# Optimization experiments

Measured on AMD Instinct MI355X. Metric: run time of the kernel, lower is better.

## Reference

```python
import jax, jax.numpy as jnp
import numpy as np

N = 100000      # nodes
E = 1600000     # edges (avg degree 16)
DIN = 48        # input features
H = 48          # hidden
DOUT = 16       # output classes


def setup_inputs() -> dict:
    key = jax.random.key(0)
    ks = jax.random.split(key, 20)
    inp = {
        "x": jax.random.normal(ks[0], (N, DIN), jnp.float32),
        "edge_index": jax.random.randint(ks[1], (2, E), 0, N, jnp.int32),
    }
    # (name, in_dim, out_dim) for the 2-layer MLP in each of 3 GINConvs + final fc
    layers = [("11", DIN, H), ("12", H, H),
              ("21", H, H), ("22", H, H),
              ("31", H, H), ("32", H, H),
              ("f1", H, H), ("f2", H, DOUT)]
    for i, (nm, din, dout) in enumerate(layers):
        inp["w" + nm] = jax.random.normal(ks[2 + i], (din, dout), jnp.float32) / np.float32(np.sqrt(din))
        inp["b" + nm] = jax.random.normal(ks[10 + i], (dout,), jnp.float32) * 0.01
    return inp


def reference(x, edge_index, w11, b11, w12, b12, w21, b21, w22, b22,
              w31, b31, w32, b32, wf1, bf1, wf2, bf2):
    src, dst = edge_index[0], edge_index[1]
    n = x.shape[0]

    def gin_conv(h, w1, b1, w2, b2):
        # scatter-sum neighbor aggregation: sum_{j in N(i)} h_j
        agg = jax.ops.segment_sum(h[src], dst, num_segments=n)  # [N, d]
        h2 = h + agg  # eps = 0 (PyG GINConv default): (1+eps)*x + agg
        h2 = jax.nn.relu(h2 @ w1 + b1)
        return jax.nn.relu(h2 @ w2 + b2)

    h = gin_conv(x, w11, b11, w12, b12)
    h = gin_conv(h, w21, b21, w22, b22)
    h = gin_conv(h, w31, b31, w32, b32)
    # final fc head: Linear -> ReLU -> Linear
    return jax.nn.relu(h @ wf1 + bf1) @ wf2 + bf2
```

## Files before the change

### kernel.cpp

```cpp
#include <hip/hip_runtime.h>

#define NN 100000
#define NE 1600000
#define D 48
#define BK_SHIFT 8
#define BK_NODES 256
#define NBK 391
#define CAP 5120
#define EPB 4096
#define NBINB 391
#define NG 1563
#define CAPG 1344
#define ST 72

typedef _Float16 f16x8 __attribute__((ext_vector_type(8)));
typedef float f32x4 __attribute__((ext_vector_type(4)));


__global__ __launch_bounds__(256) void prepbin(
    const int* __restrict__ src, const int* __restrict__ dst,
    int* __restrict__ bucketLen, int* __restrict__ arena,
    const float* __restrict__ x,
    const float* __restrict__ w11, const float* __restrict__ w12,
    const float* __restrict__ w21, const float* __restrict__ w22,
    const float* __restrict__ w31, const float* __restrict__ w32,
    const float* __restrict__ wf1, const float* __restrict__ wf2,
    _Float16* __restrict__ wp, uint4* __restrict__ outh) {
    __shared__ int sCnt[NBK];
    __shared__ int sBase[NBK];
    int b = blockIdx.x;
    int tid = threadIdx.x;
    if (b < NBINB) {
        for (int i = tid; i < NBK; i += 256) sCnt[i] = 0;
        __syncthreads();
        int e0 = b * EPB;
        int eend = e0 + EPB;
        if (eend > NE) eend = NE;
        for (int i = e0 + tid; i < eend; i += 256) atomicAdd(&sCnt[dst[i] >> BK_SHIFT], 1);
        __syncthreads();
        int rot = (b * 101) % NBK;
        for (int k = tid; k < NBK; k += 256) {
            int i = k + rot;
            if (i >= NBK) i -= NBK;
            int v = sCnt[i];
            sBase[i] = v ? atomicAdd(&bucketLen[i], v) : 0;
        }
        __syncthreads();
        for (int i = tid; i < NBK; i += 256) sCnt[i] = 0;
        __syncthreads();
        for (int i = e0 + tid; i < eend; i += 256) {
            int d = dst[i];
            int bk = d >> BK_SHIFT;
            int off = atomicAdd(&sCnt[bk], 1) + sBase[bk];
            if (off < CAP) arena[(size_t)bk * CAP + off] = ((d & (BK_NODES - 1)) << 17) | src[i];
        }
    } else if (b < NBINB + 8) {
        int l = b - NBINB;
        const float* W;
        int NL = 48;
        switch (l) {
            case 0: W = w11; break;
            case 1: W = w12; break;
            case 2: W = w21; break;
            case 3: W = w22; break;
            case 4: W = w31; break;
            case 5: W = w32; break;
            case 6: W = wf1; break;
            default: W = wf2; NL = 16; break;
        }
        _Float16* T = wp + l * 3072;
        int total = 64 * NL;
        for (int i = tid; i < total; i += 256) {
            int j = i & 7;
            int m = i >> 3;
            int g = m / NL;
            int nn = m - g * NL;
            int k = g * 8 + j;
            T[i] = (k < 48) ? (_Float16)W[k * NL + nn] : (_Float16)0.f;
        }
    } else {
        int i = (b - NBINB - 8) * 256 + tid;
        if (i < NN * 6) {
            const float4* p = (const float4*)(x + (size_t)i * 8);
            float4 a = p[0], bb = p[1];
            union { _Float16 h[8]; uint4 u; } pk;
            pk.h[0] = (_Float16)a.x; pk.h[1] = (_Float16)a.y;
            pk.h[2] = (_Float16)a.z; pk.h[3] = (_Float16)a.w;
            pk.h[4] = (_Float16)bb.x; pk.h[5] = (_Float16)bb.y;
            pk.h[6] = (_Float16)bb.z; pk.h[7] = (_Float16)bb.w;
            outh[i] = pk.u;
        }
    }
}


__global__ __launch_bounds__(256) void csr64(
    const int* __restrict__ arena, const int* __restrict__ bucketLen,
    int* __restrict__ rowptr, int* __restrict__ gEnd, int* __restrict__ colidx) {
    __shared__ int sCnt[64];
    __shared__ int sPos[64];
    int g = blockIdx.x;
    int tid = threadIdx.x;
    int parent = g >> 2;
    int quarter = g & 3;
    int plen = bucketLen[parent];
    if (plen > CAP) plen = CAP;
    const int* slice = arena + (size_t)parent * CAP;
    int gBase = g * CAPG;

    if (tid < 64) sCnt[tid] = 0;
    __syncthreads();
    for (int i = tid; i < plen; i += 256) {
        int p = slice[i];
        if ((p >> 23) == quarter) atomicAdd(&sCnt[(p >> 17) & 63], 1);
    }
    __syncthreads();
    if (tid < 64) {
        int v = sCnt[tid];
        int xx = v;
#pragma unroll
        for (int off = 1; off < 64; off <<= 1) {
            int y = __shfl_up(xx, off);
            if (tid >= off) xx += y;
        }
        int excl = xx - v;
        if (excl > CAPG) excl = CAPG;
        int node = (g << 6) + tid;
        if (node < NN) rowptr[node] = gBase + excl;
        sPos[tid] = gBase + excl;
        if (tid == 63) {
            int tot = xx > CAPG ? CAPG : xx;
            gEnd[g] = gBase + tot;
        }
    }
    __syncthreads();
    int lim = gBase + CAPG;
    for (int i = tid; i < plen; i += 256) {
        int p = slice[i];
        if ((p >> 23) == quarter) {
            int slot = atomicAdd(&sPos[(p >> 17) & 63], 1);
            if (slot < lim) colidx[slot] = p & 0x1FFFF;
        }
    }
}


__device__ __forceinline__ void mfma_layer48(
    const _Float16* __restrict__ wp, const float* __restrict__ bias,
    const _Float16* src, _Float16* dst, int lane) {
    int am = lane & 15, q = lane >> 4;
    f16x8 a0 = *(const f16x8*)(src + am * ST + q * 8);
    f16x8 a1 = *(const f16x8*)(src + am * ST + 32 + q * 8);
#pragma unroll
    for (int t = 0; t < 3; ++t) {
        f16x8 b0 = *(const f16x8*)(wp + ((q) * 48 + t * 16 + am) * 8);
        f16x8 b1 = *(const f16x8*)(wp + ((4 + q) * 48 + t * 16 + am) * 8);
        float bv = bias[t * 16 + am];
        f32x4 c = {bv, bv, bv, bv};
        c = __builtin_amdgcn_mfma_f32_16x16x32_f16(a0, b0, c, 0, 0, 0);
        c = __builtin_amdgcn_mfma_f32_16x16x32_f16(a1, b1, c, 0, 0, 0);
#pragma unroll
        for (int r = 0; r < 4; ++r) {
            float v = fmaxf(c[r], 0.f);
            dst[(q * 4 + r) * ST + t * 16 + am] = (_Float16)v;
        }
    }
}


__device__ __forceinline__ void gather_stage(const uint4* __restrict__ hin4,
                                             const int* __restrict__ rowptr,
                                             const int* __restrict__ col,
                                             int gend,
                                             _Float16* s0, _Float16* s1,
                                             int base, int wv, int lane, int n) {
    for (int i = lane; i < 16 * 3; i += 64) {
        int r = i / 3, cq = i % 3;
        *(uint4*)(s0 + r * ST + 48 + cq * 8) = make_uint4(0u, 0u, 0u, 0u);
        *(uint4*)(s1 + r * ST + 48 + cq * 8) = make_uint4(0u, 0u, 0u, 0u);
    }
    int s = lane & 7;
    int c = lane >> 3;
    bool act = (c < 6);
    int cc = act ? c : 0;
    int nb = base + wv * 16;
    for (int nl = 0; nl < 16; nl += 2) {
        int node0 = nb + nl;
        int node1 = node0 + 1;
        int r1 = wv * 16 + nl + 1;
        f16x8 acc0 = {0, 0, 0, 0, 0, 0, 0, 0};
        f16x8 acc1 = {0, 0, 0, 0, 0, 0, 0, 0};
        int e00 = 0, e01 = 0, e10 = 0, e11 = 0;
        if (node0 < n) {
            e00 = rowptr[node0];
            e01 = rowptr[node0 + 1];
        }
        if (node1 < n) {
            e10 = e01;
            e11 = (r1 == 63 || node1 == n - 1) ? gend : rowptr[node1 + 1];
        }
        if (act) {
            int ebA = e00, ebB = e10;
            while (ebA < e01 || ebB < e11) {
                int eA0 = ebA + s, eA1 = ebA + 8 + s;
                int eB0 = ebB + s, eB1 = ebB + 8 + s;
                bool okA0 = eA0 < e01, okA1 = eA1 < e01;
                bool okB0 = eB0 < e11, okB1 = eB1 < e11;
                int iA0 = col[okA0 ? eA0 : e00] & 0x1FFFF;
                int iA1 = col[okA1 ? eA1 : e00] & 0x1FFFF;
                int iB0 = col[okB0 ? eB0 : e10] & 0x1FFFF;
                int iB1 = col[okB1 ? eB1 : e10] & 0x1FFFF;
                uint4 vA0 = hin4[(size_t)iA0 * 6 + cc];
                uint4 vA1 = hin4[(size_t)iA1 * 6 + cc];
                uint4 vB0 = hin4[(size_t)iB0 * 6 + cc];
                uint4 vB1 = hin4[(size_t)iB1 * 6 + cc];
                if (!okA0) vA0 = make_uint4(0u, 0u, 0u, 0u);
                if (!okA1) vA1 = make_uint4(0u, 0u, 0u, 0u);
                if (!okB0) vB0 = make_uint4(0u, 0u, 0u, 0u);
                if (!okB1) vB1 = make_uint4(0u, 0u, 0u, 0u);
                acc0 += *(const f16x8*)&vA0;
                acc0 += *(const f16x8*)&vA1;
                acc1 += *(const f16x8*)&vB0;
                acc1 += *(const f16x8*)&vB1;
                ebA += 16;
                ebB += 16;
            }
        }
        union { f16x8 f; int i[4]; } a0, a1, bx;
        a0.f = acc0;
        a1.f = acc1;
#pragma unroll
        for (int m = 1; m <= 4; m <<= 1) {
            bx.i[0] = __shfl_xor(a0.i[0], m);
            bx.i[1] = __shfl_xor(a0.i[1], m);
            bx.i[2] = __shfl_xor(a0.i[2], m);
            bx.i[3] = __shfl_xor(a0.i[3], m);
            a0.f += bx.f;
            bx.i[0] = __shfl_xor(a1.i[0], m);
            bx.i[1] = __shfl_xor(a1.i[1], m);
            bx.i[2] = __shfl_xor(a1.i[2], m);
            bx.i[3] = __shfl_xor(a1.i[3], m);
            a1.f += bx.f;
        }
        if (s == 0 && act) {
            union { f16x8 f; uint4 u; } r0u, r1u;
            r0u.f = (f16x8){0, 0, 0, 0, 0, 0, 0, 0};
            r1u.f = (f16x8){0, 0, 0, 0, 0, 0, 0, 0};
            if (node0 < n) {
                uint4 self = hin4[(size_t)node0 * 6 + c];
                r0u.f = a0.f + *(const f16x8*)&self;
            }
            if (node1 < n) {
                uint4 self = hin4[(size_t)node1 * 6 + c];
                r1u.f = a1.f + *(const f16x8*)&self;
            }
            *(uint4*)(s0 + nl * ST + c * 8) = r0u.u;
            *(uint4*)(s0 + (nl + 1) * ST + c * 8) = r1u.u;
        }
    }
    __builtin_amdgcn_wave_barrier();
}

__global__ __launch_bounds__(256) void conv_fused(
    const uint4* __restrict__ hin4, const int* __restrict__ rowptr,
    const int* __restrict__ col, const int* __restrict__ gEnd,
    const _Float16* __restrict__ wp1, const float* __restrict__ B1,
    const _Float16* __restrict__ wp2, const float* __restrict__ B2,
    _Float16* __restrict__ hout, int n) {
    __shared__ __align__(16) _Float16 HA[2 * 64 * ST];
    int tid = threadIdx.x;
    int g = blockIdx.x;
    int base = g << 6;
    int lane = tid & 63;
    int wv = tid >> 6;
    _Float16* s0 = HA + wv * 16 * ST;
    _Float16* s1 = HA + 64 * ST + wv * 16 * ST;

    int gend = gEnd[g];

    gather_stage(hin4, rowptr, col, gend, s0, s1, base, wv, lane, n);
    mfma_layer48(wp1, B1, s0, s1, lane);
    __builtin_amdgcn_wave_barrier();

    int am = lane & 15, q = lane >> 4;
    f16x8 a0 = *(const f16x8*)(s1 + am * ST + q * 8);
    f16x8 a1 = *(const f16x8*)(s1 + am * ST + 32 + q * 8);
    int g0 = base + wv * 16;
#pragma unroll
    for (int t = 0; t < 3; ++t) {
        f16x8 b0 = *(const f16x8*)(wp2 + ((q) * 48 + t * 16 + am) * 8);
        f16x8 b1 = *(const f16x8*)(wp2 + ((4 + q) * 48 + t * 16 + am) * 8);
        float bv = B2[t * 16 + am];
        f32x4 c = {bv, bv, bv, bv};
        c = __builtin_amdgcn_mfma_f32_16x16x32_f16(a0, b0, c, 0, 0, 0);
        c = __builtin_amdgcn_mfma_f32_16x16x32_f16(a1, b1, c, 0, 0, 0);
#pragma unroll
        for (int r = 0; r < 4; ++r) {
            int node = g0 + q * 4 + r;
            if (node < n) {
                float v = fmaxf(c[r], 0.f);
                hout[(size_t)node * D + t * 16 + am] = (_Float16)v;
            }
        }
    }
}

__global__ __launch_bounds__(256) void tail_fused(
    const uint4* __restrict__ hin4, const int* __restrict__ rowptr,
    const int* __restrict__ col, const int* __restrict__ gEnd,
    const _Float16* __restrict__ wp1, const float* __restrict__ B1,
    const _Float16* __restrict__ wp2, const float* __restrict__ B2,
    const _Float16* __restrict__ wp3, const float* __restrict__ B3,
    const _Float16* __restrict__ wp4, const float* __restrict__ B4,
    float* __restrict__ out, int n) {
    __shared__ __align__(16) _Float16 HA[2 * 64 * ST];
    int tid = threadIdx.x;
    int g = blockIdx.x;
    int base = g << 6;
    int lane = tid & 63;
    int wv = tid >> 6;
    _Float16* s0 = HA + wv * 16 * ST;
    _Float16* s1 = HA + 64 * ST + wv * 16 * ST;

    int gend = gEnd[g];

    gather_stage(hin4, rowptr, col, gend, s0, s1, base, wv, lane, n);
    mfma_layer48(wp1, B1, s0, s1, lane);
    __builtin_amdgcn_wave_barrier();
    mfma_layer48(wp2, B2, s1, s0, lane);
    __builtin_amdgcn_wave_barrier();
    mfma_layer48(wp3, B3, s0, s1, lane);
    __builtin_amdgcn_wave_barrier();

    int am = lane & 15, q = lane >> 4;
    f16x8 a0 = *(const f16x8*)(s1 + am * ST + q * 8);
    f16x8 a1 = *(const f16x8*)(s1 + am * ST + 32 + q * 8);
    f16x8 b0 = *(const f16x8*)(wp4 + ((q) * 16 + am) * 8);
    f16x8 b1 = *(const f16x8*)(wp4 + ((4 + q) * 16 + am) * 8);
    float bv = B4[am];
    f32x4 c = {bv, bv, bv, bv};
    c = __builtin_amdgcn_mfma_f32_16x16x32_f16(a0, b0, c, 0, 0, 0);
    c = __builtin_amdgcn_mfma_f32_16x16x32_f16(a1, b1, c, 0, 0, 0);
    int g0 = base + wv * 16;
#pragma unroll
    for (int r = 0; r < 4; ++r) {
        int node = g0 + q * 4 + r;
        if (node < n) out[(size_t)node * 16 + am] = c[r];
    }
}


extern "C" void kernel_launch(void* const* d_in, const int* in_sizes, int n_in,
                              void* d_out, int out_size, void* d_ws, size_t ws_size,
                              hipStream_t stream) {
    const int n = NN, e = NE;
    const float* x = (const float*)d_in[0];
    const int* ei = (const int*)d_in[1];
    const int* src = ei;
    const int* dst = ei + e;
    const float* w11 = (const float*)d_in[2];
    const float* b11 = (const float*)d_in[3];
    const float* w12 = (const float*)d_in[4];
    const float* b12 = (const float*)d_in[5];
    const float* w21 = (const float*)d_in[6];
    const float* b21 = (const float*)d_in[7];
    const float* w22 = (const float*)d_in[8];
    const float* b22 = (const float*)d_in[9];
    const float* w31 = (const float*)d_in[10];
    const float* b31 = (const float*)d_in[11];
    const float* w32 = (const float*)d_in[12];
    const float* b32 = (const float*)d_in[13];
    const float* wf1 = (const float*)d_in[14];
    const float* bf1 = (const float*)d_in[15];
    const float* wf2 = (const float*)d_in[16];
    const float* bf2 = (const float*)d_in[17];
    float* out = (float*)d_out;

    uint4* HAa = (uint4*)d_ws;
    uint4* HAb = HAa + (size_t)n * 6;
    _Float16* WP = (_Float16*)(HAb + (size_t)n * 6);
    int* rowptr = (int*)(WP + 8 * 3072);
    int* gEnd = rowptr + n;
    int* colidx = gEnd + NG;
    int* arena = colidx + (size_t)NG * CAPG;
    int* bucketLen = arena + (size_t)NBK * CAP;
    size_t needed = (size_t)((char*)(bucketLen + NBK) - (char*)d_ws);
    if (needed > ws_size) return;

    const _Float16* wp11 = WP + 0 * 3072;
    const _Float16* wp12 = WP + 1 * 3072;
    const _Float16* wp21 = WP + 2 * 3072;
    const _Float16* wp22 = WP + 3 * 3072;
    const _Float16* wp31 = WP + 4 * 3072;
    const _Float16* wp32 = WP + 5 * 3072;
    const _Float16* wpf1 = WP + 6 * 3072;
    const _Float16* wpf2 = WP + 7 * 3072;

    hipMemsetAsync(bucketLen, 0, NBK * sizeof(int), stream);
    int gPB = NBINB + 8 + (n * 6 + 255) / 256;
    prepbin<<<gPB, 256, 0, stream>>>(src, dst, bucketLen, arena, x,
                                     w11, w12, w21, w22, w31, w32, wf1, wf2,
                                     WP, HAa);
    csr64<<<NG, 256, 0, stream>>>(arena, bucketLen, rowptr, gEnd, colidx);

    int gConv = NG;

    conv_fused<<<gConv, 256, 0, stream>>>(HAa, rowptr, colidx, gEnd,
                                          wp11, b11, wp12, b12, (_Float16*)HAb, n);
    conv_fused<<<gConv, 256, 0, stream>>>(HAb, rowptr, colidx, gEnd,
                                          wp21, b21, wp22, b22, (_Float16*)HAa, n);
    tail_fused<<<gConv, 256, 0, stream>>>(HAa, rowptr, colidx, gEnd,
                                          wp31, b31, wp32, b32,
                                          wpf1, bf1, wpf2, bf2, out, n);
}
```

Baseline: 271.4 us.

## Fuse CSR construction into first GIN conv kernel using LDS column list

Removes the separate csr64 kernel and builds each 64-node group's CSR slice inside the first conv kernel, keeping the column list and row offsets in shared memory for that layer's gather. The kernel still writes rowptr, gEnd and colidx to global memory for the later layers. This saves one kernel launch and the global round-trip of colidx/rowptr for layer 1. In exchange it adds about 5.6KB of LDS per block and extra block-level syncs, which may lower occupancy of the first conv.

```diff
diff --git a/kernel.cpp b/kernel.cpp
--- a/kernel.cpp
+++ b/kernel.cpp
@@ -94,57 +94,6 @@
 }
 
 
-__global__ __launch_bounds__(256) void csr64(
-    const int* __restrict__ arena, const int* __restrict__ bucketLen,
-    int* __restrict__ rowptr, int* __restrict__ gEnd, int* __restrict__ colidx) {
-    __shared__ int sCnt[64];
-    __shared__ int sPos[64];
-    int g = blockIdx.x;
-    int tid = threadIdx.x;
-    int parent = g >> 2;
-    int quarter = g & 3;
-    int plen = bucketLen[parent];
-    if (plen > CAP) plen = CAP;
-    const int* slice = arena + (size_t)parent * CAP;
-    int gBase = g * CAPG;
-
-    if (tid < 64) sCnt[tid] = 0;
-    __syncthreads();
-    for (int i = tid; i < plen; i += 256) {
-        int p = slice[i];
-        if ((p >> 23) == quarter) atomicAdd(&sCnt[(p >> 17) & 63], 1);
-    }
-    __syncthreads();
-    if (tid < 64) {
-        int v = sCnt[tid];
-        int xx = v;
-#pragma unroll
-        for (int off = 1; off < 64; off <<= 1) {
-            int y = __shfl_up(xx, off);
-            if (tid >= off) xx += y;
-        }
-        int excl = xx - v;
-        if (excl > CAPG) excl = CAPG;
-        int node = (g << 6) + tid;
-        if (node < NN) rowptr[node] = gBase + excl;
-        sPos[tid] = gBase + excl;
-        if (tid == 63) {
-            int tot = xx > CAPG ? CAPG : xx;
-            gEnd[g] = gBase + tot;
-        }
-    }
-    __syncthreads();
-    int lim = gBase + CAPG;
-    for (int i = tid; i < plen; i += 256) {
-        int p = slice[i];
-        if ((p >> 23) == quarter) {
-            int slot = atomicAdd(&sPos[(p >> 17) & 63], 1);
-            if (slot < lim) colidx[slot] = p & 0x1FFFF;
-        }
-    }
-}
-
-
 __device__ __forceinline__ void mfma_layer48(
     const _Float16* __restrict__ wp, const float* __restrict__ bias,
     const _Float16* src, _Float16* dst, int lane) {
@@ -168,12 +117,13 @@
 }
 
 
-__device__ __forceinline__ void gather_stage(const uint4* __restrict__ hin4,
-                                             const int* __restrict__ rowptr,
-                                             const int* __restrict__ col,
-                                             int gend,
-                                             _Float16* s0, _Float16* s1,
-                                             int base, int wv, int lane, int n) {
+template <bool LDSCOL>
+__device__ __forceinline__ void gather_core(const uint4* __restrict__ hin4,
+                                            const int* col,
+                                            const int* eB0s,
+                                            int gend,
+                                            _Float16* s0, _Float16* s1,
+                                            int base, int wv, int lane, int n) {
     for (int i = lane; i < 16 * 3; i += 64) {
         int r = i / 3, cq = i % 3;
         *(uint4*)(s0 + r * ST + 48 + cq * 8) = make_uint4(0u, 0u, 0u, 0u);
@@ -187,17 +137,23 @@
     for (int nl = 0; nl < 16; nl += 2) {
         int node0 = nb + nl;
         int node1 = node0 + 1;
-        int r1 = wv * 16 + nl + 1;
+        int r0 = wv * 16 + nl, r1 = r0 + 1;
         f16x8 acc0 = {0, 0, 0, 0, 0, 0, 0, 0};
         f16x8 acc1 = {0, 0, 0, 0, 0, 0, 0, 0};
-        int e00 = 0, e01 = 0, e10 = 0, e11 = 0;
-        if (node0 < n) {
-            e00 = rowptr[node0];
-            e01 = rowptr[node0 + 1];
-        }
-        if (node1 < n) {
-            e10 = e01;
-            e11 = (r1 == 63 || node1 == n - 1) ? gend : rowptr[node1 + 1];
+        int e00, e01, e10, e11;
+        if (LDSCOL) {
+            e00 = eB0s[r0]; e01 = eB0s[r0 + 1];
+            e10 = e01;      e11 = eB0s[r1 + 1];
+        } else {
+            e00 = e01 = e10 = e11 = 0;
+            if (node0 < n) {
+                e00 = eB0s[node0];
+                e01 = eB0s[node0 + 1];
+            }
+            if (node1 < n) {
+                e10 = e01;
+                e11 = (r1 == 63 || node1 == n - 1) ? gend : eB0s[node1 + 1];
+            }
         }
         if (act) {
             int ebA = e00, ebB = e10;
@@ -261,6 +217,104 @@
     __builtin_amdgcn_wave_barrier();
 }
 
+
+__device__ __forceinline__ void layer2_out(
+    const _Float16* s1, const _Float16* __restrict__ wp2,
+    const float* __restrict__ B2, _Float16* __restrict__ hout,
+    int base, int wv, int lane, int n) {
+    int am = lane & 15, q = lane >> 4;
+    f16x8 a0 = *(const f16x8*)(s1 + am * ST + q * 8);
+    f16x8 a1 = *(const f16x8*)(s1 + am * ST + 32 + q * 8);
+    int g0 = base + wv * 16;
+#pragma unroll
+    for (int t = 0; t < 3; ++t) {
+        f16x8 b0 = *(const f16x8*)(wp2 + ((q) * 48 + t * 16 + am) * 8);
+        f16x8 b1 = *(const f16x8*)(wp2 + ((4 + q) * 48 + t * 16 + am) * 8);
+        float bv = B2[t * 16 + am];
+        f32x4 c = {bv, bv, bv, bv};
+        c = __builtin_amdgcn_mfma_f32_16x16x32_f16(a0, b0, c, 0, 0, 0);
+        c = __builtin_amdgcn_mfma_f32_16x16x32_f16(a1, b1, c, 0, 0, 0);
+#pragma unroll
+        for (int r = 0; r < 4; ++r) {
+            int node = g0 + q * 4 + r;
+            if (node < n) {
+                float v = fmaxf(c[r], 0.f);
+                hout[(size_t)node * D + t * 16 + am] = (_Float16)v;
+            }
+        }
+    }
+}
+
+__global__ __launch_bounds__(256) void conv1_fused(
+    const uint4* __restrict__ hin4, const int* __restrict__ arena,
+    const int* __restrict__ bucketLen,
+    int* __restrict__ rowptr, int* __restrict__ gEnd, int* __restrict__ colidx,
+    const _Float16* __restrict__ wp1, const float* __restrict__ B1,
+    const _Float16* __restrict__ wp2, const float* __restrict__ B2,
+    _Float16* __restrict__ hout, int n) {
+    __shared__ __align__(16) _Float16 HA[2 * 64 * ST];
+    __shared__ int sList[CAPG];
+    __shared__ int sCnt[64];
+    __shared__ int sPos[64];
+    __shared__ int sBase[65];
+    int tid = threadIdx.x;
+    int g = blockIdx.x;
+    int base = g << 6;
+    int lane = tid & 63;
+    int wv = tid >> 6;
+    _Float16* s0 = HA + wv * 16 * ST;
+    _Float16* s1 = HA + 64 * ST + wv * 16 * ST;
+
+    int parent = g >> 2;
+    int quarter = g & 3;
+    int plen = bucketLen[parent];
+    if (plen > CAP) plen = CAP;
+    const int* slice = arena + (size_t)parent * CAP;
+    if (tid < 64) sCnt[tid] = 0;
+    __syncthreads();
+    for (int i = tid; i < plen; i += 256) {
+        int p = slice[i];
+        if ((p >> 23) == quarter) atomicAdd(&sCnt[(p >> 17) & 63], 1);
+    }
+    __syncthreads();
+    if (tid < 64) {
+        int v = sCnt[tid];
+        int xx = v;
+#pragma unroll
+        for (int off = 1; off < 64; off <<= 1) {
+            int y = __shfl_up(xx, off);
+            if (tid >= off) xx += y;
+        }
+        int excl = xx - v;
+        if (excl > CAPG) excl = CAPG;
+        sBase[tid] = excl;
+        sPos[tid] = excl;
+        int node = base + tid;
+        if (node < NN) rowptr[node] = g * CAPG + excl;
+        if (tid == 63) {
+            int tot = xx > CAPG ? CAPG : xx;
+            sBase[64] = tot;
+            gEnd[g] = g * CAPG + tot;
+        }
+    }
+    __syncthreads();
+    for (int i = tid; i < plen; i += 256) {
+        int p = slice[i];
+        if ((p >> 23) == quarter) {
+            int slot = atomicAdd(&sPos[(p >> 17) & 63], 1);
+            if (slot < CAPG) sList[slot] = p & 0x1FFFF;
+        }
+    }
+    __syncthreads();
+    int tot = sBase[64];
+    for (int i = tid; i < tot; i += 256) colidx[g * CAPG + i] = sList[i];
+
+    gather_core<true>(hin4, sList, sBase, 0, s0, s1, base, wv, lane, n);
+    mfma_layer48(wp1, B1, s0, s1, lane);
+    __builtin_amdgcn_wave_barrier();
+    layer2_out(s1, wp2, B2, hout, base, wv, lane, n);
+}
+
 __global__ __launch_bounds__(256) void conv_fused(
     const uint4* __restrict__ hin4, const int* __restrict__ rowptr,
     const int* __restrict__ col, const int* __restrict__ gEnd,
@@ -277,32 +331,10 @@
     _Float16* s1 = HA + 64 * ST + wv * 16 * ST;
 
     int gend = gEnd[g];
-
-    gather_stage(hin4, rowptr, col, gend, s0, s1, base, wv, lane, n);
+    gather_core<false>(hin4, col, rowptr, gend, s0, s1, base, wv, lane, n);
     mfma_layer48(wp1, B1, s0, s1, lane);
     __builtin_amdgcn_wave_barrier();
-
-    int am = lane & 15, q = lane >> 4;
-    f16x8 a0 = *(const f16x8*)(s1 + am * ST + q * 8);
-    f16x8 a1 = *(const f16x8*)(s1 + am * ST + 32 + q * 8);
-    int g0 = base + wv * 16;
-#pragma unroll
-    for (int t = 0; t < 3; ++t) {
-        f16x8 b0 = *(const f16x8*)(wp2 + ((q) * 48 + t * 16 + am) * 8);
-        f16x8 b1 = *(const f16x8*)(wp2 + ((4 + q) * 48 + t * 16 + am) * 8);
-        float bv = B2[t * 16 + am];
-        f32x4 c = {bv, bv, bv, bv};
-        c = __builtin_amdgcn_mfma_f32_16x16x32_f16(a0, b0, c, 0, 0, 0);
-        c = __builtin_amdgcn_mfma_f32_16x16x32_f16(a1, b1, c, 0, 0, 0);
-#pragma unroll
-        for (int r = 0; r < 4; ++r) {
-            int node = g0 + q * 4 + r;
-            if (node < n) {
-                float v = fmaxf(c[r], 0.f);
-                hout[(size_t)node * D + t * 16 + am] = (_Float16)v;
-            }
-        }
-    }
+    layer2_out(s1, wp2, B2, hout, base, wv, lane, n);
 }
 
 __global__ __launch_bounds__(256) void tail_fused(
@@ -323,8 +355,7 @@
     _Float16* s1 = HA + 64 * ST + wv * 16 * ST;
 
     int gend = gEnd[g];
-
-    gather_stage(hin4, rowptr, col, gend, s0, s1, base, wv, lane, n);
+    gather_core<false>(hin4, col, rowptr, gend, s0, s1, base, wv, lane, n);
     mfma_layer48(wp1, B1, s0, s1, lane);
     __builtin_amdgcn_wave_barrier();
     mfma_layer48(wp2, B2, s1, s0, lane);
@@ -401,12 +432,12 @@
     prepbin<<<gPB, 256, 0, stream>>>(src, dst, bucketLen, arena, x,
                                      w11, w12, w21, w22, w31, w32, wf1, wf2,
                                      WP, HAa);
-    csr64<<<NG, 256, 0, stream>>>(arena, bucketLen, rowptr, gEnd, colidx);
 
     int gConv = NG;
 
-    conv_fused<<<gConv, 256, 0, stream>>>(HAa, rowptr, colidx, gEnd,
-                                          wp11, b11, wp12, b12, (_Float16*)HAb, n);
+    conv1_fused<<<gConv, 256, 0, stream>>>(HAa, arena, bucketLen,
+                                           rowptr, gEnd, colidx,
+                                           wp11, b11, wp12, b12, (_Float16*)HAb, n);
     conv_fused<<<gConv, 256, 0, stream>>>(HAb, rowptr, colidx, gEnd,
                                           wp21, b21, wp22, b22, (_Float16*)HAa, n);
     tail_fused<<<gConv, 256, 0, stream>>>(HAa, rowptr, colidx, gEnd,
```

Measured after the change: 279.8 us. +3.1%, slower.
